# Performance work log

Hardware: AMD Instinct MI355X
Metric: run time of the kernel (lower is better)

Reference implementation:

```python
import jax, jax.numpy as jnp
import numpy as np

B, T, F, H = 16, 512, 32, 128
EPS = 1e-5


def _layer_norm(y, g, b):
    mu = jnp.mean(y, axis=-1, keepdims=True)
    var = jnp.mean(jnp.square(y - mu), axis=-1, keepdims=True)
    return (y - mu) * jax.lax.rsqrt(var + EPS) * g + b


def setup_inputs() -> dict:
    key = jax.random.key(0)
    ks = jax.random.split(key, 16)
    s = 0.1  # small param scale
    return {
        "x": jax.random.normal(ks[0], (B, T, F), jnp.float32),
        # weight GRN (input_size == hidden == F, skip is Identity)
        "wg_fc1_w": jax.random.normal(ks[1], (F, F), jnp.float32) * s,
        "wg_fc1_b": jnp.zeros((F,), jnp.float32),
        "wg_fc2_w": jax.random.normal(ks[2], (2 * F, F), jnp.float32) * s,
        "wg_fc2_b": jnp.zeros((2 * F,), jnp.float32),
        "wg_ln_g": jnp.ones((F,), jnp.float32),
        "wg_ln_b": jnp.zeros((F,), jnp.float32),
        # per-feature GRNs (input_size=1 -> hidden H), batched over F
        "f_fc1_w": jax.random.normal(ks[3], (F, H), jnp.float32) * s,   # torch Linear(1,H).weight squeezed
        "f_fc1_b": jax.random.normal(ks[4], (F, H), jnp.float32) * s,
        "f_fc2_w": jax.random.normal(ks[5], (F, 2 * H, H), jnp.float32) * s,
        "f_fc2_b": jax.random.normal(ks[6], (F, 2 * H), jnp.float32) * s,
        "f_skip_w": jax.random.normal(ks[7], (F, H), jnp.float32) * s,  # Linear(1,H).weight squeezed
        "f_skip_b": jax.random.normal(ks[8], (F, H), jnp.float32) * s,
        "f_ln_g": jnp.ones((F, H), jnp.float32),
        "f_ln_b": jnp.zeros((F, H), jnp.float32),
    }


def reference(x, wg_fc1_w, wg_fc1_b, wg_fc2_w, wg_fc2_b, wg_ln_g, wg_ln_b,
              f_fc1_w, f_fc1_b, f_fc2_w, f_fc2_b, f_skip_w, f_skip_b,
              f_ln_g, f_ln_b):
    # --- weight GRN over the feature axis: [B,T,F] -> [B,T,F] ---
    h = jax.nn.elu(jnp.einsum('btf,gf->btg', x, wg_fc1_w) + wg_fc1_b)
    h2 = jnp.einsum('btg,kg->btk', h, wg_fc2_w) + wg_fc2_b  # [B,T,2F]
    a, g = jnp.split(h2, 2, axis=-1)
    glu = a * jax.nn.sigmoid(g)
    weights = jax.nn.softmax(_layer_norm(x + glu, wg_ln_g, wg_ln_b), axis=-1)  # [B,T,F]

    # --- all F per-feature GRNs batched (input width 1) ---
    xe = x[..., None]                                   # [B,T,F,1]
    h = jax.nn.elu(xe * f_fc1_w + f_fc1_b)              # [B,T,F,H]
    h2 = jnp.einsum('btfh,fgh->btfg', h, f_fc2_w) + f_fc2_b  # [B,T,F,2H]
    a, g = jnp.split(h2, 2, axis=-1)
    glu = a * jax.nn.sigmoid(g)                         # [B,T,F,H]
    res = xe * f_skip_w + f_skip_b                      # [B,T,F,H]
    y = _layer_norm(res + glu, f_ln_g, f_ln_b)          # per-feature LN params [F,H]

    # --- softmax-weighted combine ---
    return jnp.einsum('btf,btfh->bth', weights, y)      # [B,T,H]
```

## Files before the change

### kernel.cpp

```cpp
#include <hip/hip_runtime.h>
#include <cstdint>
#include <cstddef>

#define EPS 1e-5f

typedef float    f4    __attribute__((ext_vector_type(4)));
typedef _Float16 half8 __attribute__((ext_vector_type(8)));
typedef _Float16 half4 __attribute__((ext_vector_type(4)));

#define S_XS 33
#define LOG2E 1.44269504088896f

#define GLD_LDS16(gp, lp)                                        \
    __builtin_amdgcn_global_load_lds(                            \
        (const __attribute__((address_space(1))) void*)(gp),     \
        (__attribute__((address_space(3))) void*)(lp), 16, 0, 0)

__device__ __forceinline__ float fexp(float x)  { return __builtin_amdgcn_exp2f(x * LOG2E); }
__device__ __forceinline__ float frcp(float x)  { return __builtin_amdgcn_rcpf(x); }
__device__ __forceinline__ float frsq(float x)  { return __builtin_amdgcn_rsqf(x); }
__device__ __forceinline__ float fsig(float g)  { return frcp(1.f + __builtin_amdgcn_exp2f(g * -LOG2E)); }
__device__ __forceinline__ float felu(float t)  { return t > 0.f ? t : fexp(t) - 1.f; }

__global__ __launch_bounds__(256) void k_prep(
    const float* __restrict__ in_w2, _Float16* __restrict__ w2c,
    const float* __restrict__ x, const float* __restrict__ w1,
    const float* __restrict__ b1, const float* __restrict__ w2,
    const float* __restrict__ b2, const float* __restrict__ lng,
    const float* __restrict__ lnb,
    float* __restrict__ x_t, float* __restrict__ wts_t,
    float* __restrict__ outp)
{
    __shared__ float w1s[32 * S_XS];
    __shared__ float w2s[64 * S_XS];
    __shared__ float xsW[32 * S_XS];
    __shared__ float ytile[32 * S_XS];

    const int bid = blockIdx.x;
    const int tid = threadIdx.x;

    if (bid < 512) {
        int t = bid * 256 + tid;
        int q  = t & 3;
        int g  = (t >> 2) & 255;
        int fk = t >> 10;
        int f = fk >> 2, kq = fk & 3;
        const float* ip = in_w2 + ((size_t)f * 256 + g) * 128 + kq * 32 + q * 8;
        f4 v0 = *(const f4*)ip, v1 = *(const f4*)(ip + 4);
        half8 h;
        #pragma unroll
        for (int i = 0; i < 4; ++i) { h[i] = (_Float16)v0[i]; h[4 + i] = (_Float16)v1[i]; }
        *(half8*)(w2c + (size_t)fk * 8192 + q * 2048 + g * 8) = h;
        return;
    }

    if (bid >= 768) {
        int t = (bid - 768) * 256 + tid;
        f4 z; z[0] = 0.f; z[1] = 0.f; z[2] = 0.f; z[3] = 0.f;
        for (int i = t; i < 262144; i += 4096)
            *(f4*)(outp + (size_t)i * 4) = z;
        return;
    }

    const int lane = tid & 63;
    const int f = lane & 31;
    const int wv = tid >> 6;
    const int row0 = (bid - 512) * 32;

    for (int i = tid; i < 1024; i += 256) {
        int r = i >> 5, c = i & 31;
        w1s[r * S_XS + c] = w1[i];
        xsW[r * S_XS + c] = x[(size_t)row0 * 32 + i];
    }
    for (int i = tid; i < 2048; i += 256) {
        int r = i >> 5, c = i & 31;
        w2s[r * S_XS + c] = w2[i];
    }
    const float b1f = b1[f], b2a = b2[f], b2g = b2[f + 32];
    const float lgf = lng[f], lbf = lnb[f];
    __syncthreads();

    for (int rr = 0; rr < 8; ++rr) {
        const int r = wv * 8 + rr;
        float acc = b1f;
        #pragma unroll
        for (int k = 0; k < 32; ++k)
            acc = fmaf(w1s[f * S_XS + k], xsW[r * S_XS + k], acc);
        float hval = felu(acc);

        float a = b2a, g = b2g;
        #pragma unroll
        for (int k = 0; k < 32; ++k) {
            float hk = __shfl(hval, k, 64);
            a = fmaf(w2s[f * S_XS + k], hk, a);
            g = fmaf(w2s[(f + 32) * S_XS + k], hk, g);
        }
        float xv = xsW[r * S_XS + f];
        float v = xv + a * fsig(g);

        float s = v;
        #pragma unroll
        for (int o = 1; o < 64; o <<= 1) s += __shfl_xor(s, o, 64);
        float mu = s * (1.f / 64.f);
        float d = v - mu;
        float sq = d * d;
        #pragma unroll
        for (int o = 1; o < 64; o <<= 1) sq += __shfl_xor(sq, o, 64);
        float y = d * frsq(sq * (1.f / 64.f) + EPS) * lgf + lbf;

        float m = y;
        #pragma unroll
        for (int o = 1; o < 64; o <<= 1) m = fmaxf(m, __shfl_xor(m, o, 64));
        float e = fexp(y - m);
        float se = e;
        #pragma unroll
        for (int o = 1; o < 64; o <<= 1) se += __shfl_xor(se, o, 64);
        if (lane < 32) ytile[r * S_XS + f] = e * 2.f * frcp(se);
    }
    __syncthreads();
    for (int i = tid; i < 1024; i += 256) {
        int ff = i >> 5, r = i & 31;
        x_t[(size_t)ff * 8192 + row0 + r]   = xsW[r * S_XS + ff];
        wts_t[(size_t)ff * 8192 + row0 + r] = ytile[r * S_XS + ff];
    }
}

__global__ __launch_bounds__(256, 3) void k_main(
    const _Float16* __restrict__ w2c,
    const float* __restrict__ x_t,
    const float* __restrict__ wts_t,
    const float* __restrict__ fc1w, const float* __restrict__ fc1b,
    const float* __restrict__ fc2b,
    const float* __restrict__ skw, const float* __restrict__ skb,
    const float* __restrict__ lng, const float* __restrict__ lnb,
    float* __restrict__ out)
{
    __shared__ __align__(16) _Float16 bchunk[2][8192];

    const int tid = threadIdx.x;
    const int fbase = (blockIdx.x >> 7) * 4;
    const int row0 = (blockIdx.x & 127) * 64;

    const int lane = tid & 63;
    const int wv = tid >> 6;
    const int l15 = lane & 15;
    const int q = lane >> 4;
    const int boff = q * 2048 + l15 * 8;

    auto stage = [&](int c) {
        const _Float16* gp = w2c + ((size_t)(fbase + (c >> 2)) * 4 + (c & 3)) * 8192;
        #pragma unroll
        for (int r = 0; r < 4; ++r)
            GLD_LDS16(gp + (r * 256 + tid) * 8,
                      &bchunk[c & 1][(r * 256 + tid) * 8]);
    };

    float out_acc[8][4];
    #pragma unroll
    for (int nt = 0; nt < 8; ++nt)
        #pragma unroll
        for (int rg = 0; rg < 4; ++rg) out_acc[nt][rg] = 0.f;

    stage(0);
    __syncthreads();

    int c = 0;
    for (int fi = 0; fi < 4; ++fi) {
        const int f = fbase + fi;
        const float* xcol = x_t + (size_t)f * 8192 + row0 + wv * 16;
        const float* wcol = wts_t + (size_t)f * 8192 + row0 + wv * 16;
        const float xvA = xcol[l15];

        half8 A[4];
        #pragma unroll
        for (int kq = 0; kq < 4; ++kq) {
            const float* wp = fc1w + f * 128 + kq * 32 + 8 * q;
            const float* bp = fc1b + f * 128 + kq * 32 + 8 * q;
            f4 w0 = *(const f4*)wp, w1v = *(const f4*)(wp + 4);
            f4 b0 = *(const f4*)bp, b1v = *(const f4*)(bp + 4);
            #pragma unroll
            for (int j = 0; j < 4; ++j) {
                A[kq][j]     = (_Float16)felu(fmaf(xvA, w0[j], b0[j]));
                A[kq][4 + j] = (_Float16)felu(fmaf(xvA, w1v[j], b1v[j]));
            }
        }

        f4 acc[16];
        #pragma unroll
        for (int nt = 0; nt < 8; ++nt) {
            const int h = nt * 16 + l15;
            float ba = fc2b[f * 256 + h];
            float bg = fc2b[f * 256 + 128 + h];
            #pragma unroll
            for (int rg = 0; rg < 4; ++rg) { acc[nt][rg] = ba; acc[nt + 8][rg] = bg; }
        }

        #pragma unroll
        for (int kq = 0; kq < 4; ++kq, ++c) {
            if (c + 1 < 16) stage(c + 1);
            const _Float16* bb = &bchunk[c & 1][boff];
            #pragma unroll
            for (int nt = 0; nt < 16; ++nt) {
                half8 B = *(const half8*)(bb + nt * 128);
                acc[nt] = __builtin_amdgcn_mfma_f32_16x16x32_f16(A[kq], B, acc[nt], 0, 0, 0);
            }
            __syncthreads();
        }

        f4 xr = *(const f4*)(xcol + 4 * q);
        f4 wr = *(const f4*)(wcol + 4 * q);
        float s[4] = {0.f, 0.f, 0.f, 0.f}, sq[4] = {0.f, 0.f, 0.f, 0.f};
        #pragma unroll
        for (int nt = 0; nt < 8; ++nt) {
            const int h = nt * 16 + l15;
            float sw = skw[f * 128 + h];
            float sb = skb[f * 128 + h];
            #pragma unroll
            for (int rg = 0; rg < 4; ++rg) {
                float a = acc[nt][rg];
                float g = acc[nt + 8][rg];
                float val = fmaf(xr[rg], sw, sb) + a * fsig(g);
                acc[nt][rg] = val;
                s[rg] += val;
                sq[rg] = fmaf(val, val, sq[rg]);
            }
        }
        #pragma unroll
        for (int o = 1; o < 16; o <<= 1) {
            #pragma unroll
            for (int rg = 0; rg < 4; ++rg) {
                s[rg] += __shfl_xor(s[rg], o, 64);
                sq[rg] += __shfl_xor(sq[rg], o, 64);
            }
        }
        float mu[4], c1[4];
        #pragma unroll
        for (int rg = 0; rg < 4; ++rg) {
            mu[rg] = s[rg] * (1.f / 128.f);
            float var = sq[rg] * (1.f / 128.f) - mu[rg] * mu[rg];
            c1[rg] = wr[rg] * frsq(fmaxf(var, 0.f) + EPS);
        }
        #pragma unroll
        for (int nt = 0; nt < 8; ++nt) {
            const int h = nt * 16 + l15;
            float lg = lng[f * 128 + h];
            float lb = lnb[f * 128 + h];
            #pragma unroll
            for (int rg = 0; rg < 4; ++rg) {
                float u = (acc[nt][rg] - mu[rg]) * c1[rg];
                out_acc[nt][rg] = fmaf(u, lg, fmaf(wr[rg], lb, out_acc[nt][rg]));
            }
        }
    }

    #pragma unroll
    for (int nt = 0; nt < 8; ++nt) {
        #pragma unroll
        for (int rg = 0; rg < 4; ++rg) {
            const int r = row0 + wv * 16 + 4 * q + rg;
            atomicAdd(&out[(size_t)r * 128 + nt * 16 + l15], out_acc[nt][rg]);
        }
    }
}

extern "C" void kernel_launch(void* const* d_in, const int* in_sizes, int n_in,
                              void* d_out, int out_size, void* d_ws, size_t ws_size,
                              hipStream_t stream) {
    const float* x     = (const float*)d_in[0];
    const float* wg1w  = (const float*)d_in[1];
    const float* wg1b  = (const float*)d_in[2];
    const float* wg2w  = (const float*)d_in[3];
    const float* wg2b  = (const float*)d_in[4];
    const float* wglng = (const float*)d_in[5];
    const float* wglnb = (const float*)d_in[6];
    const float* fc1w  = (const float*)d_in[7];
    const float* fc1b  = (const float*)d_in[8];
    const float* fc2w  = (const float*)d_in[9];
    const float* fc2b  = (const float*)d_in[10];
    const float* skw   = (const float*)d_in[11];
    const float* skb   = (const float*)d_in[12];
    const float* lng   = (const float*)d_in[13];
    const float* lnb   = (const float*)d_in[14];
    float* out = (float*)d_out;

    char* ws = (char*)d_ws;
    _Float16* w2c = (_Float16*)ws;
    float* x_t    = (float*)(ws + (2u << 20));
    float* wts_t  = (float*)(ws + (3u << 20));

    k_prep<<<dim3(784), dim3(256), 0, stream>>>(fc2w, w2c, x, wg1w, wg1b,
                                                wg2w, wg2b, wglng, wglnb,
                                                x_t, wts_t, out);
    k_main<<<dim3(1024), dim3(256), 0, stream>>>(w2c, x_t, wts_t, fc1w, fc1b,
                                                 fc2b, skw, skb, lng, lnb, out);
}
```

Measured before the change: 165.2 us.

## Split waves over row and hidden halves, load fc2 weights directly from global

Drops the LDS double-buffered staging of fp16 fc2 weights through global_load_lds. Each wave now loads its B fragments straight from global memory. Waves are re-tiled into a 2x2 grid: each covers 32 rows (two A fragments) and half of the hidden outputs, so every loaded B fragment feeds two MFMAs. The split of the hidden dimension means the LayerNorm sums must be combined across wave pairs through a small shared array with extra barriers. The trade is less LDS traffic and fewer per-chunk barriers against global-load latency that is no longer hidden by prefetch.

```diff
diff --git a/kernel.cpp b/kernel.cpp
--- a/kernel.cpp
+++ b/kernel.cpp
@@ -6,15 +6,9 @@
 
 typedef float    f4    __attribute__((ext_vector_type(4)));
 typedef _Float16 half8 __attribute__((ext_vector_type(8)));
-typedef _Float16 half4 __attribute__((ext_vector_type(4)));
 
 #define S_XS 33
 #define LOG2E 1.44269504088896f
-
-#define GLD_LDS16(gp, lp)                                        \
-    __builtin_amdgcn_global_load_lds(                            \
-        (const __attribute__((address_space(1))) void*)(gp),     \
-        (__attribute__((address_space(3))) void*)(lp), 16, 0, 0)
 
 __device__ __forceinline__ float fexp(float x)  { return __builtin_amdgcn_exp2f(x * LOG2E); }
 __device__ __forceinline__ float frcp(float x)  { return __builtin_amdgcn_rcpf(x); }
@@ -135,7 +129,7 @@
     const float* __restrict__ lng, const float* __restrict__ lnb,
     float* __restrict__ out)
 {
-    __shared__ __align__(16) _Float16 bchunk[2][8192];
+    __shared__ float red[2][2][4][4][2][2];
 
     const int tid = threadIdx.x;
     const int fbase = (blockIdx.x >> 7) * 4;
@@ -143,35 +137,27 @@
 
     const int lane = tid & 63;
     const int wv = tid >> 6;
+    const int rowhalf = wv >> 1;
+    const int hhalf = wv & 1;
     const int l15 = lane & 15;
     const int q = lane >> 4;
-    const int boff = q * 2048 + l15 * 8;
-
-    auto stage = [&](int c) {
-        const _Float16* gp = w2c + ((size_t)(fbase + (c >> 2)) * 4 + (c & 3)) * 8192;
-        #pragma unroll
-        for (int r = 0; r < 4; ++r)
-            GLD_LDS16(gp + (r * 256 + tid) * 8,
-                      &bchunk[c & 1][(r * 256 + tid) * 8]);
-    };
-
-    float out_acc[8][4];
+
+    float out_acc[2][4][4];
     #pragma unroll
-    for (int nt = 0; nt < 8; ++nt)
-        #pragma unroll
-        for (int rg = 0; rg < 4; ++rg) out_acc[nt][rg] = 0.f;
-
-    stage(0);
-    __syncthreads();
-
-    int c = 0;
+    for (int g2 = 0; g2 < 2; ++g2)
+        #pragma unroll
+        for (int nt = 0; nt < 4; ++nt)
+            #pragma unroll
+            for (int rg = 0; rg < 4; ++rg) out_acc[g2][nt][rg] = 0.f;
+
     for (int fi = 0; fi < 4; ++fi) {
         const int f = fbase + fi;
-        const float* xcol = x_t + (size_t)f * 8192 + row0 + wv * 16;
-        const float* wcol = wts_t + (size_t)f * 8192 + row0 + wv * 16;
-        const float xvA = xcol[l15];
-
-        half8 A[4];
+        const float* xcol = x_t + (size_t)f * 8192 + row0 + rowhalf * 32;
+        const float* wcol = wts_t + (size_t)f * 8192 + row0 + rowhalf * 32;
+        const float xv0 = xcol[l15];
+        const float xv1 = xcol[16 + l15];
+
+        half8 A0[4], A1[4];
         #pragma unroll
         for (int kq = 0; kq < 4; ++kq) {
             const float* wp = fc1w + f * 128 + kq * 32 + 8 * q;
@@ -180,85 +166,142 @@
             f4 b0 = *(const f4*)bp, b1v = *(const f4*)(bp + 4);
             #pragma unroll
             for (int j = 0; j < 4; ++j) {
-                A[kq][j]     = (_Float16)felu(fmaf(xvA, w0[j], b0[j]));
-                A[kq][4 + j] = (_Float16)felu(fmaf(xvA, w1v[j], b1v[j]));
-            }
-        }
-
-        f4 acc[16];
-        #pragma unroll
-        for (int nt = 0; nt < 8; ++nt) {
-            const int h = nt * 16 + l15;
+                A0[kq][j]     = (_Float16)felu(fmaf(xv0, w0[j], b0[j]));
+                A0[kq][4 + j] = (_Float16)felu(fmaf(xv0, w1v[j], b1v[j]));
+                A1[kq][j]     = (_Float16)felu(fmaf(xv1, w0[j], b0[j]));
+                A1[kq][4 + j] = (_Float16)felu(fmaf(xv1, w1v[j], b1v[j]));
+            }
+        }
+
+        f4 accA0[4], accG0[4], accA1[4], accG1[4];
+        #pragma unroll
+        for (int nt = 0; nt < 4; ++nt) {
+            const int h = hhalf * 64 + nt * 16 + l15;
             float ba = fc2b[f * 256 + h];
             float bg = fc2b[f * 256 + 128 + h];
             #pragma unroll
-            for (int rg = 0; rg < 4; ++rg) { acc[nt][rg] = ba; acc[nt + 8][rg] = bg; }
-        }
-
-        #pragma unroll
-        for (int kq = 0; kq < 4; ++kq, ++c) {
-            if (c + 1 < 16) stage(c + 1);
-            const _Float16* bb = &bchunk[c & 1][boff];
-            #pragma unroll
-            for (int nt = 0; nt < 16; ++nt) {
-                half8 B = *(const half8*)(bb + nt * 128);
-                acc[nt] = __builtin_amdgcn_mfma_f32_16x16x32_f16(A[kq], B, acc[nt], 0, 0, 0);
-            }
-            __syncthreads();
-        }
-
-        f4 xr = *(const f4*)(xcol + 4 * q);
-        f4 wr = *(const f4*)(wcol + 4 * q);
-        float s[4] = {0.f, 0.f, 0.f, 0.f}, sq[4] = {0.f, 0.f, 0.f, 0.f};
-        #pragma unroll
-        for (int nt = 0; nt < 8; ++nt) {
-            const int h = nt * 16 + l15;
+            for (int rg = 0; rg < 4; ++rg) {
+                accA0[nt][rg] = ba; accA1[nt][rg] = ba;
+                accG0[nt][rg] = bg; accG1[nt][rg] = bg;
+            }
+        }
+
+        const _Float16* bp0 = w2c + (size_t)f * 4 * 8192
+                            + q * 2048 + hhalf * 512 + l15 * 8;
+
+        #pragma unroll
+        for (int kq = 0; kq < 4; ++kq) {
+            const _Float16* bp = bp0 + kq * 8192;
+            half8 B0 = *(const half8*)(bp);
+            half8 B1 = *(const half8*)(bp + 128);
+            half8 B2 = *(const half8*)(bp + 256);
+            half8 B3 = *(const half8*)(bp + 384);
+            accA0[0] = __builtin_amdgcn_mfma_f32_16x16x32_f16(A0[kq], B0, accA0[0], 0, 0, 0);
+            accA1[0] = __builtin_amdgcn_mfma_f32_16x16x32_f16(A1[kq], B0, accA1[0], 0, 0, 0);
+            accA0[1] = __builtin_amdgcn_mfma_f32_16x16x32_f16(A0[kq], B1, accA0[1], 0, 0, 0);
+            accA1[1] = __builtin_amdgcn_mfma_f32_16x16x32_f16(A1[kq], B1, accA1[1], 0, 0, 0);
+            accA0[2] = __builtin_amdgcn_mfma_f32_16x16x32_f16(A0[kq], B2, accA0[2], 0, 0, 0);
+            accA1[2] = __builtin_amdgcn_mfma_f32_16x16x32_f16(A1[kq], B2, accA1[2], 0, 0, 0);
+            accA0[3] = __builtin_amdgcn_mfma_f32_16x16x32_f16(A0[kq], B3, accA0[3], 0, 0, 0);
+            accA1[3] = __builtin_amdgcn_mfma_f32_16x16x32_f16(A1[kq], B3, accA1[3], 0, 0, 0);
+            half8 G0 = *(const half8*)(bp + 1024);
+            half8 G1 = *(const half8*)(bp + 1152);
+            half8 G2 = *(const half8*)(bp + 1280);
+            half8 G3 = *(const half8*)(bp + 1408);
+            accG0[0] = __builtin_amdgcn_mfma_f32_16x16x32_f16(A0[kq], G0, accG0[0], 0, 0, 0);
+            accG1[0] = __builtin_amdgcn_mfma_f32_16x16x32_f16(A1[kq], G0, accG1[0], 0, 0, 0);
+            accG0[1] = __builtin_amdgcn_mfma_f32_16x16x32_f16(A0[kq], G1, accG0[1], 0, 0, 0);
+            accG1[1] = __builtin_amdgcn_mfma_f32_16x16x32_f16(A1[kq], G1, accG1[1], 0, 0, 0);
+            accG0[2] = __builtin_amdgcn_mfma_f32_16x16x32_f16(A0[kq], G2, accG0[2], 0, 0, 0);
+            accG1[2] = __builtin_amdgcn_mfma_f32_16x16x32_f16(A1[kq], G2, accG1[2], 0, 0, 0);
+            accG0[3] = __builtin_amdgcn_mfma_f32_16x16x32_f16(A0[kq], G3, accG0[3], 0, 0, 0);
+            accG1[3] = __builtin_amdgcn_mfma_f32_16x16x32_f16(A1[kq], G3, accG1[3], 0, 0, 0);
+        }
+
+        float s0[4], sq0[4], s1[4], sq1[4];
+        #pragma unroll
+        for (int rg = 0; rg < 4; ++rg) { s0[rg] = 0.f; sq0[rg] = 0.f; s1[rg] = 0.f; sq1[rg] = 0.f; }
+
+        f4 xr0 = *(const f4*)(xcol + 4 * q);
+        f4 xr1 = *(const f4*)(xcol + 16 + 4 * q);
+        #pragma unroll
+        for (int nt = 0; nt < 4; ++nt) {
+            const int h = hhalf * 64 + nt * 16 + l15;
             float sw = skw[f * 128 + h];
             float sb = skb[f * 128 + h];
             #pragma unroll
             for (int rg = 0; rg < 4; ++rg) {
-                float a = acc[nt][rg];
-                float g = acc[nt + 8][rg];
-                float val = fmaf(xr[rg], sw, sb) + a * fsig(g);
-                acc[nt][rg] = val;
-                s[rg] += val;
-                sq[rg] = fmaf(val, val, sq[rg]);
+                float v0 = fmaf(xr0[rg], sw, sb) + accA0[nt][rg] * fsig(accG0[nt][rg]);
+                float v1 = fmaf(xr1[rg], sw, sb) + accA1[nt][rg] * fsig(accG1[nt][rg]);
+                accA0[nt][rg] = v0;
+                accA1[nt][rg] = v1;
+                s0[rg] += v0; sq0[rg] = fmaf(v0, v0, sq0[rg]);
+                s1[rg] += v1; sq1[rg] = fmaf(v1, v1, sq1[rg]);
             }
         }
         #pragma unroll
         for (int o = 1; o < 16; o <<= 1) {
             #pragma unroll
             for (int rg = 0; rg < 4; ++rg) {
-                s[rg] += __shfl_xor(s[rg], o, 64);
-                sq[rg] += __shfl_xor(sq[rg], o, 64);
-            }
-        }
-        float mu[4], c1[4];
+                s0[rg] += __shfl_xor(s0[rg], o, 64);
+                sq0[rg] += __shfl_xor(sq0[rg], o, 64);
+                s1[rg] += __shfl_xor(s1[rg], o, 64);
+                sq1[rg] += __shfl_xor(sq1[rg], o, 64);
+            }
+        }
+        if (l15 == 0) {
+            #pragma unroll
+            for (int rg = 0; rg < 4; ++rg) {
+                red[rowhalf][0][q][rg][hhalf][0] = s0[rg];
+                red[rowhalf][0][q][rg][hhalf][1] = sq0[rg];
+                red[rowhalf][1][q][rg][hhalf][0] = s1[rg];
+                red[rowhalf][1][q][rg][hhalf][1] = sq1[rg];
+            }
+        }
+        __syncthreads();
+
+        f4 wr0 = *(const f4*)(wcol + 4 * q);
+        f4 wr1 = *(const f4*)(wcol + 16 + 4 * q);
+        float mu0[4], c10[4], mu1[4], c11[4];
         #pragma unroll
         for (int rg = 0; rg < 4; ++rg) {
-            mu[rg] = s[rg] * (1.f / 128.f);
-            float var = sq[rg] * (1.f / 128.f) - mu[rg] * mu[rg];
-            c1[rg] = wr[rg] * frsq(fmaxf(var, 0.f) + EPS);
-        }
-        #pragma unroll
-        for (int nt = 0; nt < 8; ++nt) {
-            const int h = nt * 16 + l15;
+            float st0 = s0[rg] + red[rowhalf][0][q][rg][hhalf ^ 1][0];
+            float qt0 = sq0[rg] + red[rowhalf][0][q][rg][hhalf ^ 1][1];
+            float st1 = s1[rg] + red[rowhalf][1][q][rg][hhalf ^ 1][0];
+            float qt1 = sq1[rg] + red[rowhalf][1][q][rg][hhalf ^ 1][1];
+            mu0[rg] = st0 * (1.f / 128.f);
+            mu1[rg] = st1 * (1.f / 128.f);
+            float var0 = qt0 * (1.f / 128.f) - mu0[rg] * mu0[rg];
+            float var1 = qt1 * (1.f / 128.f) - mu1[rg] * mu1[rg];
+            c10[rg] = wr0[rg] * frsq(fmaxf(var0, 0.f) + EPS);
+            c11[rg] = wr1[rg] * frsq(fmaxf(var1, 0.f) + EPS);
+        }
+        #pragma unroll
+        for (int nt = 0; nt < 4; ++nt) {
+            const int h = hhalf * 64 + nt * 16 + l15;
             float lg = lng[f * 128 + h];
             float lb = lnb[f * 128 + h];
             #pragma unroll
             for (int rg = 0; rg < 4; ++rg) {
-                float u = (acc[nt][rg] - mu[rg]) * c1[rg];
-                out_acc[nt][rg] = fmaf(u, lg, fmaf(wr[rg], lb, out_acc[nt][rg]));
-            }
-        }
+                float u0 = (accA0[nt][rg] - mu0[rg]) * c10[rg];
+                float u1 = (accA1[nt][rg] - mu1[rg]) * c11[rg];
+                out_acc[0][nt][rg] = fmaf(u0, lg, fmaf(wr0[rg], lb, out_acc[0][nt][rg]));
+                out_acc[1][nt][rg] = fmaf(u1, lg, fmaf(wr1[rg], lb, out_acc[1][nt][rg]));
+            }
+        }
+        __syncthreads();
     }
 
     #pragma unroll
-    for (int nt = 0; nt < 8; ++nt) {
-        #pragma unroll
-        for (int rg = 0; rg < 4; ++rg) {
-            const int r = row0 + wv * 16 + 4 * q + rg;
-            atomicAdd(&out[(size_t)r * 128 + nt * 16 + l15], out_acc[nt][rg]);
+    for (int g2 = 0; g2 < 2; ++g2) {
+        #pragma unroll
+        for (int nt = 0; nt < 4; ++nt) {
+            #pragma unroll
+            for (int rg = 0; rg < 4; ++rg) {
+                const int r = row0 + rowhalf * 32 + g2 * 16 + 4 * q + rg;
+                atomicAdd(&out[(size_t)r * 128 + hhalf * 64 + nt * 16 + l15],
+                          out_acc[g2][nt][rg]);
+            }
         }
     }
 }
```

Result: slower. 179.2 us (+8.4%).
